# Kernel tuning notes

Hardware: AMD Instinct MI355X
Metric: run time of the kernel (lower is better)

The kernel has to match this reference:

```python
import jax, jax.numpy as jnp
import numpy as np

B, C, S, H, W = 2, 128, 64, 128, 512
MID = 32
EPS = 1e-5


def layer_norm(x, g, b):
    m = jnp.mean(x, axis=-1, keepdims=True)
    v = jnp.var(x, axis=-1, keepdims=True)
    return (x - m) / jnp.sqrt(v + EPS) * g + b


def generate_y_for_attn(s, y, u):
    # y: [B, Cy, H, W], u: [B, s, s] int indices into W (clamped)
    b, cy, h, w = y.shape
    u = jnp.clip(u, 0, w - 1)
    yr = y.reshape(b, cy * h, w)
    idx = u.reshape(b, s * s)
    g = jax.vmap(lambda m, i: m[:, i])(yr, idx)          # [B, Cy*H, s^2]
    return g.reshape(b, cy, h, s * s).transpose(0, 3, 2, 1)  # [B, s^2, H, Cy]


def setup_inputs():
    key = jax.random.key(0)
    ks = jax.random.split(key, 10)
    lim = 1.0 / np.sqrt(C)
    return {
        "sat_x": jax.random.normal(ks[0], (B, C, S, S), jnp.float32),
        "grd_x": jax.random.normal(ks[1], (B, C, H, W), jnp.float32),
        "grd_height": jax.random.normal(ks[2], (B, 1, H, W), jnp.float32),
        "u": jax.random.randint(ks[3], (B, S, S), 0, W, jnp.int32),
        "ln_q_g": jnp.ones((C,), jnp.float32),
        "ln_q_b": jnp.zeros((C,), jnp.float32),
        "wq": jax.random.uniform(ks[4], (C, MID), jnp.float32, -lim, lim),
        "bq": jax.random.uniform(ks[5], (MID,), jnp.float32, -lim, lim),
        "ln_k_g": jnp.ones((C,), jnp.float32),
        "ln_k_b": jnp.zeros((C,), jnp.float32),
        "wk": jax.random.uniform(ks[6], (C, MID), jnp.float32, -lim, lim),
        "bk": jax.random.uniform(ks[7], (MID,), jnp.float32, -lim, lim),
    }


def reference(sat_x, grd_x, grd_height, u, ln_q_g, ln_q_b, wq, bq, ln_k_g, ln_k_b, wk, bk):
    b, c, s, _ = sat_x.shape
    scale = MID ** (-0.5)
    y_attn = generate_y_for_attn(s, grd_x, u)        # [B, S^2, H, C]
    v_attn = generate_y_for_attn(s, grd_height, u)   # [B, S^2, H, 1]
    x = sat_x.reshape(b, c, s * s).transpose(0, 2, 1)  # [B, M, C]
    q = layer_norm(x, ln_q_g, ln_q_b) @ wq + bq        # [B, M, 32]
    k = layer_norm(y_attn, ln_k_g, ln_k_b) @ wk + bk   # [B, M, H, 32]
    dot = scale * jnp.einsum("bmd,bmnd->bmn", q, k)    # [B, M, H]
    att = jax.nn.softmax(dot, axis=-1)
    a = jnp.sum(att[..., None] * v_attn, axis=-2)      # [B, M, 1]
    return a.transpose(0, 2, 1).reshape(b, 1, s, s)
```

## Files before the change

kernel.cpp:

```cpp
#include <hip/hip_runtime.h>
#include <math.h>

#define B_   2
#define C_   128
#define S_   64
#define H_   128
#define W_   512
#define M_   (S_ * S_)
#define MID_ 32
#define EPS_ 1e-5f
#define CAP_ 192

#define KBLK (B_ * H_ * (W_ / 64))
#define QBLK (B_ * (M_ / 64))
#define NTILE (KBLK + QBLK)
#define PGRID 1024
#define OBLK 4

typedef __attribute__((ext_vector_type(8))) short short8;
typedef __attribute__((ext_vector_type(4))) float floatx4;

__device__ __forceinline__ unsigned bfpair(float a, float b) {
    unsigned ua = __float_as_uint(a); ua += 0x7FFFu + ((ua >> 16) & 1u);
    unsigned ub = __float_as_uint(b); ub += 0x7FFFu + ((ub >> 16) & 1u);
    return (ua >> 16) | (ub & 0xFFFF0000u);
}

__global__ __launch_bounds__(256) void prep_kernel(
    const float* __restrict__ ln_k_g, const float* __restrict__ ln_k_b,
    const float* __restrict__ wk, const float* __restrict__ bk,
    const float* __restrict__ ln_q_g, const float* __restrict__ ln_q_b,
    const float* __restrict__ wq, const float* __restrict__ bq,
    float* __restrict__ prepbuf,
    short* __restrict__ wfrag,
    int* __restrict__ counts,
    int* __restrict__ ocount)
{
    const int tid = threadIdx.x;
    const int blk = blockIdx.x;
    const float* g    = blk ? ln_q_g : ln_k_g;
    const float* bl   = blk ? ln_q_b : ln_k_b;
    const float* wt   = blk ? wq     : wk;
    const float* bias = blk ? bq     : bk;

    __shared__ float pa[256], pb[256];

    float a = 0.f, c2 = 0.f;
#pragma unroll
    for (int k = 0; k < 16; ++k) {
        const int idx = tid + 256 * k;
        const float wv = wt[idx];
        const int c = idx >> 5;
        a  = fmaf(g[c],  wv, a);
        c2 = fmaf(bl[c], wv, c2);
    }
    pa[tid] = a; pb[tid] = c2;

    if (blk == 0) {
        ((int4*)counts)[tid] = make_int4(0, 0, 0, 0);
        if (tid == 0) *ocount = 0;
    }
    __syncthreads();

    if (tid < 32) {
        float s = 0.f, t = 0.f;
#pragma unroll
        for (int r = 0; r < 8; ++r) { s += pa[tid + 32 * r]; t += pb[tid + 32 * r]; }
        prepbuf[blk * 64 + tid]      = s;
        prepbuf[blk * 64 + 32 + tid] = t + bias[tid];
    }

    short* whiT = wfrag + blk * 8192;
    short* wloT = whiT + 4096;
#pragma unroll
    for (int e = 0; e < 16; ++e) {
        const int idx = tid * 16 + e;
        const int i    = idx & 7;
        const int ln   = (idx >> 3) & 63;
        const int kk   = (idx >> 9) & 3;
        const int jt   = idx >> 11;
        const int c = kk * 32 + (ln >> 4) * 8 + i;
        const int j = jt * 16 + (ln & 15);
        const float wp = g[c] * wt[c * MID_ + j];
        const unsigned bbits = __float_as_uint(wp);
        const unsigned hb = bbits & 0xFFFF0000u;
        whiT[idx] = (short)(hb >> 16);
        const float r = wp - __uint_as_float(hb);
        wloT[idx] = (short)(__float_as_uint(r) >> 16);
    }
}

struct Geo {
    const float* xcol;
    size_t xstr;
    int b, h, pos0;
    bool is_k;
};

__device__ __forceinline__ Geo tile_geo(int t, const float* __restrict__ grd_x,
                                        const float* __restrict__ sat_x) {
    Geo ge;
    ge.is_k = (t < KBLK);
    if (ge.is_k) {
        const int wchunk = t & 7;
        ge.h    = (t >> 3) & (H_ - 1);
        ge.b    = t >> 10;
        ge.pos0 = wchunk * 64;
        ge.xcol = grd_x + ((size_t)ge.b * C_ * H_ + ge.h) * W_ + ge.pos0;
        ge.xstr = (size_t)H_ * W_;
    } else {
        const int qblk = t - KBLK;
        ge.b    = qblk >> 6;
        ge.h    = 0;
        ge.pos0 = (qblk & 63) * 64;
        ge.xcol = sat_x + (size_t)ge.b * C_ * M_ + ge.pos0;
        ge.xstr = (size_t)M_;
    }
    return ge;
}

__device__ __forceinline__ void issue_dma(const Geo& ge, float* xs, int lane, int wv) {
    const int swz  = (wv >> 1) << 4;
    const float* gsrc = ge.xcol + (size_t)(lane >> 4) * ge.xstr
                               + (((lane & 15) * 4) ^ swz);
#pragma unroll
    for (int r = 0; r < 8; ++r) {
        const float* src = gsrc + (size_t)(r * 16 + wv * 4) * ge.xstr;
        float* dst = xs + (r * 16 + wv * 4) * 64;
        __builtin_amdgcn_global_load_lds(
            (const __attribute__((address_space(1))) unsigned int*)src,
            (__attribute__((address_space(3))) unsigned int*)dst,
            16, 0, 0);
    }
}

__global__ __launch_bounds__(256) void proj_kernel(
    const float* __restrict__ grd_x,
    const float* __restrict__ sat_x,
    const float* __restrict__ prepbuf,
    const short* __restrict__ wfrag,
    const int*   __restrict__ u,
    unsigned short* __restrict__ kwb,
    float* __restrict__ qv,
    int* __restrict__ counts,
    int* __restrict__ bucket,
    int* __restrict__ ocount,
    int* __restrict__ olist)
{
    __shared__ float xs[C_ * 64];

    const int tid  = threadIdx.x;
    const int lane = tid & 63;
    const int wv   = __builtin_amdgcn_readfirstlane(tid >> 6);
    const int quad = lane >> 4;
    const int l16  = lane & 15;
    const int blk  = blockIdx.x;

    issue_dma(tile_geo(blk, grd_x, sat_x), xs, lane, wv);

    for (int t = blk; t < NTILE; t += PGRID) {
        const Geo ge = tile_geo(t, grd_x, sat_x);
        const bool is_k = ge.is_k;
        const int pos = ge.pos0 + wv * 16 + l16;

        const short* whiT = wfrag + (is_k ? 0 : 8192);
        const short* wloT = whiT + 4096;
        short8 ahi[2][4], alo[2][4];
#pragma unroll
        for (int jt = 0; jt < 2; ++jt)
#pragma unroll
            for (int kk = 0; kk < 4; ++kk) {
                const int off = ((jt * 4 + kk) * 64 + lane) * 8;
                ahi[jt][kk] = *(const short8*)(whiT + off);
                alo[jt][kk] = *(const short8*)(wloT + off);
            }

        const int setoff = is_k ? 0 : 64;
        const float4 gw0 = *(const float4*)(prepbuf + setoff + quad * 4);
        const float4 bw0 = *(const float4*)(prepbuf + setoff + 32 + quad * 4);
        const float4 gw1 = *(const float4*)(prepbuf + setoff + 16 + quad * 4);
        const float4 bw1 = *(const float4*)(prepbuf + setoff + 48 + quad * 4);

        __syncthreads();

        floatx4 acc0 = {0.f, 0.f, 0.f, 0.f};
        floatx4 acc1 = {0.f, 0.f, 0.f, 0.f};
        float p1 = 0.f, p2 = 0.f;

        const int rpos = (wv * 16 + l16) ^ ((quad & 1) << 4);
        const float* xsl = xs + quad * 8 * 64 + rpos;

#pragma unroll
        for (int kk = 0; kk < 4; ++kk) {
            const float* xk = xsl + kk * 32 * 64;
            union { short8 v; unsigned u[4]; } bhi, blo;
#pragma unroll
            for (int e = 0; e < 4; ++e) {
                const float x0 = xk[(2 * e)     * 64];
                const float x1 = xk[(2 * e + 1) * 64];
                p1 += x0 + x1;
                p2 = fmaf(x0, x0, p2);
                p2 = fmaf(x1, x1, p2);
                const unsigned b0 = __float_as_uint(x0);
                const unsigned b1 = __float_as_uint(x1);
                bhi.u[e] = (b1 & 0xFFFF0000u) | (b0 >> 16);
                const float r0 = x0 - __uint_as_float(b0 & 0xFFFF0000u);
                const float r1 = x1 - __uint_as_float(b1 & 0xFFFF0000u);
                blo.u[e] = (__float_as_uint(r1) & 0xFFFF0000u) |
                           (__float_as_uint(r0) >> 16);
            }
            acc0 = __builtin_amdgcn_mfma_f32_16x16x32_bf16(ahi[0][kk], bhi.v, acc0, 0, 0, 0);
            acc1 = __builtin_amdgcn_mfma_f32_16x16x32_bf16(ahi[1][kk], bhi.v, acc1, 0, 0, 0);
            acc0 = __builtin_amdgcn_mfma_f32_16x16x32_bf16(ahi[0][kk], blo.v, acc0, 0, 0, 0);
            acc1 = __builtin_amdgcn_mfma_f32_16x16x32_bf16(ahi[1][kk], blo.v, acc1, 0, 0, 0);
            acc0 = __builtin_amdgcn_mfma_f32_16x16x32_bf16(alo[0][kk], bhi.v, acc0, 0, 0, 0);
            acc1 = __builtin_amdgcn_mfma_f32_16x16x32_bf16(alo[1][kk], bhi.v, acc1, 0, 0, 0);
        }

        __syncthreads();
        if (t + PGRID < NTILE)
            issue_dma(tile_geo(t + PGRID, grd_x, sat_x), xs, lane, wv);

        p1 += __shfl_xor(p1, 16, 64);
        p1 += __shfl_xor(p1, 32, 64);
        p2 += __shfl_xor(p2, 16, 64);
        p2 += __shfl_xor(p2, 32, 64);
        const float mean = p1 * (1.f / C_);
        const float rstd = rsqrtf(fmaf(-mean, mean, p2 * (1.f / C_)) + EPS_);

        const float o0x = fmaf(rstd, fmaf(-mean, gw0.x, acc0[0]), bw0.x);
        const float o0y = fmaf(rstd, fmaf(-mean, gw0.y, acc0[1]), bw0.y);
        const float o0z = fmaf(rstd, fmaf(-mean, gw0.z, acc0[2]), bw0.z);
        const float o0w = fmaf(rstd, fmaf(-mean, gw0.w, acc0[3]), bw0.w);
        const float o1x = fmaf(rstd, fmaf(-mean, gw1.x, acc1[0]), bw1.x);
        const float o1y = fmaf(rstd, fmaf(-mean, gw1.y, acc1[1]), bw1.y);
        const float o1z = fmaf(rstd, fmaf(-mean, gw1.z, acc1[2]), bw1.z);
        const float o1w = fmaf(rstd, fmaf(-mean, gw1.w, acc1[3]), bw1.w);

        if (is_k) {
            unsigned short* orow = kwb + (((size_t)ge.b * W_ + pos) * H_ + ge.h) * MID_;
            uint2 u0, u1;
            u0.x = bfpair(o0x, o0y); u0.y = bfpair(o0z, o0w);
            u1.x = bfpair(o1x, o1y); u1.y = bfpair(o1z, o1w);
            *(uint2*)(orow + quad * 4)      = u0;
            *(uint2*)(orow + 16 + quad * 4) = u1;
        } else {
            float* orow = qv + ((size_t)ge.b * M_ + pos) * MID_;
            *(float4*)(orow + quad * 4)      = make_float4(o0x, o0y, o0z, o0w);
            *(float4*)(orow + 16 + quad * 4) = make_float4(o1x, o1y, o1z, o1w);
            if (quad == 0) {
                const int bm = ge.b * M_ + pos;
                int w = u[bm];
                w = min(max(w, 0), W_ - 1);
                const int bw = ge.b * W_ + w;
                const int p = atomicAdd(&counts[bw], 1);
                if (p < CAP_) bucket[bw * CAP_ + p] = bm;
                else          olist[atomicAdd(ocount, 1)] = bm;
            }
        }
    }
}

__global__ __launch_bounds__(256) void battn_kernel(
    const float* __restrict__ qv,
    const unsigned short* __restrict__ kwb,
    const float* __restrict__ gh,
    const int*   __restrict__ u,
    const int*   __restrict__ counts,
    const int*   __restrict__ bucket,
    const int*   __restrict__ ocount,
    const int*   __restrict__ olist,
    float* __restrict__ out)
{
    const int blk  = blockIdx.x;
    const int tid  = threadIdx.x;
    const int lane = tid & 63;
    const int wv   = __builtin_amdgcn_readfirstlane(tid >> 6);
    const float sc = 0.17677669529663687f;

    if (blk >= B_ * W_) {
        const int nof = min(*ocount, B_ * M_);
        const int gwv = (blk - B_ * W_) * 4 + wv;
        for (int i = gwv; i < nof; i += OBLK * 4) {
            const int bm = __builtin_amdgcn_readfirstlane(olist[i]);
            const int b  = bm >> 12;
            int w = u[bm];
            w = min(max(w, 0), W_ - 1);
            const unsigned short* kr = kwb + ((size_t)b * W_ + w) * H_ * MID_;
            const float* qr = qv + (size_t)bm * MID_;
            float sq[MID_];
#pragma unroll
            for (int j = 0; j < MID_; ++j) sq[j] = qr[j];
            float d0 = 0.f, d1 = 0.f;
#pragma unroll
            for (int j = 0; j < MID_; ++j) {
                d0 = fmaf(sq[j], __uint_as_float((unsigned)kr[lane * MID_ + j] << 16), d0);
                d1 = fmaf(sq[j], __uint_as_float((unsigned)kr[(lane + 64) * MID_ + j] << 16), d1);
            }
            d0 *= sc; d1 *= sc;
            float mx = fmaxf(d0, d1);
#pragma unroll
            for (int o = 32; o > 0; o >>= 1) mx = fmaxf(mx, __shfl_xor(mx, o, 64));
            const float v0 = gh[((size_t)b * H_ + lane) * W_ + w];
            const float v1 = gh[((size_t)b * H_ + lane + 64) * W_ + w];
            const float e0 = __expf(d0 - mx);
            const float e1 = __expf(d1 - mx);
            float s   = e0 + e1;
            float svv = fmaf(e0, v0, e1 * v1);
#pragma unroll
            for (int o = 32; o > 0; o >>= 1) {
                s   += __shfl_xor(s,   o, 64);
                svv += __shfl_xor(svv, o, 64);
            }
            if (lane == 0) out[bm] = svv / s;
        }
        return;
    }

    const int n = min(counts[blk], CAP_);
    if (wv >= n) return;

    const int b = blk >> 9;
    const int w = blk & (W_ - 1);

    const uint4* k4 = (const uint4*)(kwb + (size_t)blk * H_ * MID_);
    float ka[32], kb[32];
#pragma unroll
    for (int t = 0; t < 4; ++t) {
        const uint4 ua = k4[lane * 4 + t];
        const uint4 ub = k4[(lane + 64) * 4 + t];
        ka[t*8+0] = __uint_as_float(ua.x << 16); ka[t*8+1] = __uint_as_float(ua.x & 0xFFFF0000u);
        ka[t*8+2] = __uint_as_float(ua.y << 16); ka[t*8+3] = __uint_as_float(ua.y & 0xFFFF0000u);
        ka[t*8+4] = __uint_as_float(ua.z << 16); ka[t*8+5] = __uint_as_float(ua.z & 0xFFFF0000u);
        ka[t*8+6] = __uint_as_float(ua.w << 16); ka[t*8+7] = __uint_as_float(ua.w & 0xFFFF0000u);
        kb[t*8+0] = __uint_as_float(ub.x << 16); kb[t*8+1] = __uint_as_float(ub.x & 0xFFFF0000u);
        kb[t*8+2] = __uint_as_float(ub.y << 16); kb[t*8+3] = __uint_as_float(ub.y & 0xFFFF0000u);
        kb[t*8+4] = __uint_as_float(ub.z << 16); kb[t*8+5] = __uint_as_float(ub.z & 0xFFFF0000u);
        kb[t*8+6] = __uint_as_float(ub.w << 16); kb[t*8+7] = __uint_as_float(ub.w & 0xFFFF0000u);
    }

    const float v0 = gh[((size_t)b * H_ + lane) * W_ + w];
    const float v1 = gh[((size_t)b * H_ + lane + 64) * W_ + w];

    const int* bkt = bucket + (size_t)blk * CAP_;

    for (int i = wv; i < n; i += 4) {
        const int bm = __builtin_amdgcn_readfirstlane(bkt[i]);
        const float* qr = qv + (size_t)bm * MID_;
        float sq[MID_];
#pragma unroll
        for (int j = 0; j < MID_; ++j) sq[j] = qr[j];

        float d0 = 0.f, d1 = 0.f;
#pragma unroll
        for (int j = 0; j < MID_; ++j) {
            d0 = fmaf(sq[j], ka[j], d0);
            d1 = fmaf(sq[j], kb[j], d1);
        }
        d0 *= sc; d1 *= sc;

        float mx = fmaxf(d0, d1);
#pragma unroll
        for (int o = 32; o > 0; o >>= 1) mx = fmaxf(mx, __shfl_xor(mx, o, 64));

        const float e0 = __expf(d0 - mx);
        const float e1 = __expf(d1 - mx);
        float s   = e0 + e1;
        float svv = fmaf(e0, v0, e1 * v1);
#pragma unroll
        for (int o = 32; o > 0; o >>= 1) {
            s   += __shfl_xor(s,   o, 64);
            svv += __shfl_xor(svv, o, 64);
        }

        if (lane == 0) out[bm] = svv / s;
    }
}

extern "C" void kernel_launch(void* const* d_in, const int* in_sizes, int n_in,
                              void* d_out, int out_size, void* d_ws, size_t ws_size,
                              hipStream_t stream) {
    const float* sat_x      = (const float*)d_in[0];
    const float* grd_x      = (const float*)d_in[1];
    const float* grd_height = (const float*)d_in[2];
    const int*   u          = (const int*)d_in[3];
    const float* ln_q_g     = (const float*)d_in[4];
    const float* ln_q_b     = (const float*)d_in[5];
    const float* wq         = (const float*)d_in[6];
    const float* bq         = (const float*)d_in[7];
    const float* ln_k_g     = (const float*)d_in[8];
    const float* ln_k_b     = (const float*)d_in[9];
    const float* wk         = (const float*)d_in[10];
    const float* bk         = (const float*)d_in[11];

    float* out = (float*)d_out;

    char* ws = (char*)d_ws;
    unsigned short* kwb = (unsigned short*)ws;
    float* q       = (float*)(ws + (size_t)8  * 1024 * 1024);
    int*   counts  = (int*)  (ws + (size_t)9  * 1024 * 1024);
    int*   ocount  = (int*)  (ws + (size_t)9  * 1024 * 1024 + 4096);
    int*   bucket  = (int*)  (ws + (size_t)9  * 1024 * 1024 + 8192);
    int*   olist   = bucket + B_ * W_ * CAP_;
    float* prepbuf = (float*)(ws + (size_t)10 * 1024 * 1024);
    short* wfrag   = (short*)(ws + (size_t)10 * 1024 * 1024 + 4096);

    prep_kernel<<<2, 256, 0, stream>>>(
        ln_k_g, ln_k_b, wk, bk, ln_q_g, ln_q_b, wq, bq,
        prepbuf, wfrag, counts, ocount);
    proj_kernel<<<PGRID, 256, 0, stream>>>(
        grd_x, sat_x, prepbuf, wfrag, u, kwb, q, counts, bucket, ocount, olist);
    battn_kernel<<<B_ * W_ + OBLK, 256, 0, stream>>>(
        q, kwb, grd_height, u, counts, bucket, ocount, olist, out);
}
```

Before: 135.5 us.

## Fold weight prep into projection kernel and launch one block per tile

```diff
diff --git a/kernel.cpp b/kernel.cpp
--- a/kernel.cpp
+++ b/kernel.cpp
@@ -14,7 +14,6 @@
 #define KBLK (B_ * H_ * (W_ / 64))
 #define QBLK (B_ * (M_ / 64))
 #define NTILE (KBLK + QBLK)
-#define PGRID 1024
 #define OBLK 4
 
 typedef __attribute__((ext_vector_type(8))) short short8;
@@ -24,70 +23,6 @@
     unsigned ua = __float_as_uint(a); ua += 0x7FFFu + ((ua >> 16) & 1u);
     unsigned ub = __float_as_uint(b); ub += 0x7FFFu + ((ub >> 16) & 1u);
     return (ua >> 16) | (ub & 0xFFFF0000u);
-}
-
-__global__ __launch_bounds__(256) void prep_kernel(
-    const float* __restrict__ ln_k_g, const float* __restrict__ ln_k_b,
-    const float* __restrict__ wk, const float* __restrict__ bk,
-    const float* __restrict__ ln_q_g, const float* __restrict__ ln_q_b,
-    const float* __restrict__ wq, const float* __restrict__ bq,
-    float* __restrict__ prepbuf,
-    short* __restrict__ wfrag,
-    int* __restrict__ counts,
-    int* __restrict__ ocount)
-{
-    const int tid = threadIdx.x;
-    const int blk = blockIdx.x;
-    const float* g    = blk ? ln_q_g : ln_k_g;
-    const float* bl   = blk ? ln_q_b : ln_k_b;
-    const float* wt   = blk ? wq     : wk;
-    const float* bias = blk ? bq     : bk;
-
-    __shared__ float pa[256], pb[256];
-
-    float a = 0.f, c2 = 0.f;
-#pragma unroll
-    for (int k = 0; k < 16; ++k) {
-        const int idx = tid + 256 * k;
-        const float wv = wt[idx];
-        const int c = idx >> 5;
-        a  = fmaf(g[c],  wv, a);
-        c2 = fmaf(bl[c], wv, c2);
-    }
-    pa[tid] = a; pb[tid] = c2;
-
-    if (blk == 0) {
-        ((int4*)counts)[tid] = make_int4(0, 0, 0, 0);
-        if (tid == 0) *ocount = 0;
-    }
-    __syncthreads();
-
-    if (tid < 32) {
-        float s = 0.f, t = 0.f;
-#pragma unroll
-        for (int r = 0; r < 8; ++r) { s += pa[tid + 32 * r]; t += pb[tid + 32 * r]; }
-        prepbuf[blk * 64 + tid]      = s;
-        prepbuf[blk * 64 + 32 + tid] = t + bias[tid];
-    }
-
-    short* whiT = wfrag + blk * 8192;
-    short* wloT = whiT + 4096;
-#pragma unroll
-    for (int e = 0; e < 16; ++e) {
-        const int idx = tid * 16 + e;
-        const int i    = idx & 7;
-        const int ln   = (idx >> 3) & 63;
-        const int kk   = (idx >> 9) & 3;
-        const int jt   = idx >> 11;
-        const int c = kk * 32 + (ln >> 4) * 8 + i;
-        const int j = jt * 16 + (ln & 15);
-        const float wp = g[c] * wt[c * MID_ + j];
-        const unsigned bbits = __float_as_uint(wp);
-        const unsigned hb = bbits & 0xFFFF0000u;
-        whiT[idx] = (short)(hb >> 16);
-        const float r = wp - __uint_as_float(hb);
-        wloT[idx] = (short)(__float_as_uint(r) >> 16);
-    }
 }
 
 struct Geo {
@@ -137,8 +72,10 @@
 __global__ __launch_bounds__(256) void proj_kernel(
     const float* __restrict__ grd_x,
     const float* __restrict__ sat_x,
-    const float* __restrict__ prepbuf,
-    const short* __restrict__ wfrag,
+    const float* __restrict__ ln_k_g, const float* __restrict__ ln_k_b,
+    const float* __restrict__ wk, const float* __restrict__ bk,
+    const float* __restrict__ ln_q_g, const float* __restrict__ ln_q_b,
+    const float* __restrict__ wq, const float* __restrict__ bq,
     const int*   __restrict__ u,
     unsigned short* __restrict__ kwb,
     float* __restrict__ qv,
@@ -155,108 +92,136 @@
     const int quad = lane >> 4;
     const int l16  = lane & 15;
     const int blk  = blockIdx.x;
-
-    issue_dma(tile_geo(blk, grd_x, sat_x), xs, lane, wv);
-
-    for (int t = blk; t < NTILE; t += PGRID) {
-        const Geo ge = tile_geo(t, grd_x, sat_x);
-        const bool is_k = ge.is_k;
-        const int pos = ge.pos0 + wv * 16 + l16;
-
-        const short* whiT = wfrag + (is_k ? 0 : 8192);
-        const short* wloT = whiT + 4096;
-        short8 ahi[2][4], alo[2][4];
-#pragma unroll
-        for (int jt = 0; jt < 2; ++jt)
-#pragma unroll
-            for (int kk = 0; kk < 4; ++kk) {
-                const int off = ((jt * 4 + kk) * 64 + lane) * 8;
-                ahi[jt][kk] = *(const short8*)(whiT + off);
-                alo[jt][kk] = *(const short8*)(wloT + off);
+    const bool is_k = (blk < KBLK);
+
+    const Geo ge = tile_geo(blk, grd_x, sat_x);
+    const int pos = ge.pos0 + wv * 16 + l16;
+
+    issue_dma(ge, xs, lane, wv);
+
+    const float* g    = is_k ? ln_k_g : ln_q_g;
+    const float* beta = is_k ? ln_k_b : ln_q_b;
+    const float* wt   = is_k ? wk     : wq;
+    const float* bias = is_k ? bk     : bq;
+
+    short8 ahi[2][4], alo[2][4];
+    float gwp0 = 0.f, gwp1 = 0.f, bwp0 = 0.f, bwp1 = 0.f;
+#pragma unroll
+    for (int kk = 0; kk < 4; ++kk) {
+#pragma unroll
+        for (int i = 0; i < 8; ++i) {
+            const int c   = kk * 32 + quad * 8 + i;
+            const float gc = g[c];
+            const float bc = beta[c];
+            {
+                const float w0 = wt[c * MID_ + l16];
+                const float wp = gc * w0;
+                const unsigned hb = __float_as_uint(wp) & 0xFFFF0000u;
+                ahi[0][kk][i] = (short)(hb >> 16);
+                const float r = wp - __uint_as_float(hb);
+                alo[0][kk][i] = (short)(__float_as_uint(r) >> 16);
+                gwp0 += wp;
+                bwp0 = fmaf(bc, w0, bwp0);
             }
-
-        const int setoff = is_k ? 0 : 64;
-        const float4 gw0 = *(const float4*)(prepbuf + setoff + quad * 4);
-        const float4 bw0 = *(const float4*)(prepbuf + setoff + 32 + quad * 4);
-        const float4 gw1 = *(const float4*)(prepbuf + setoff + 16 + quad * 4);
-        const float4 bw1 = *(const float4*)(prepbuf + setoff + 48 + quad * 4);
-
-        __syncthreads();
-
-        floatx4 acc0 = {0.f, 0.f, 0.f, 0.f};
-        floatx4 acc1 = {0.f, 0.f, 0.f, 0.f};
-        float p1 = 0.f, p2 = 0.f;
-
-        const int rpos = (wv * 16 + l16) ^ ((quad & 1) << 4);
-        const float* xsl = xs + quad * 8 * 64 + rpos;
-
-#pragma unroll
-        for (int kk = 0; kk < 4; ++kk) {
-            const float* xk = xsl + kk * 32 * 64;
-            union { short8 v; unsigned u[4]; } bhi, blo;
-#pragma unroll
-            for (int e = 0; e < 4; ++e) {
-                const float x0 = xk[(2 * e)     * 64];
-                const float x1 = xk[(2 * e + 1) * 64];
-                p1 += x0 + x1;
-                p2 = fmaf(x0, x0, p2);
-                p2 = fmaf(x1, x1, p2);
-                const unsigned b0 = __float_as_uint(x0);
-                const unsigned b1 = __float_as_uint(x1);
-                bhi.u[e] = (b1 & 0xFFFF0000u) | (b0 >> 16);
-                const float r0 = x0 - __uint_as_float(b0 & 0xFFFF0000u);
-                const float r1 = x1 - __uint_as_float(b1 & 0xFFFF0000u);
-                blo.u[e] = (__float_as_uint(r1) & 0xFFFF0000u) |
-                           (__float_as_uint(r0) >> 16);
+            {
+                const float w1 = wt[c * MID_ + 16 + l16];
+                const float wp = gc * w1;
+                const unsigned hb = __float_as_uint(wp) & 0xFFFF0000u;
+                ahi[1][kk][i] = (short)(hb >> 16);
+                const float r = wp - __uint_as_float(hb);
+                alo[1][kk][i] = (short)(__float_as_uint(r) >> 16);
+                gwp1 += wp;
+                bwp1 = fmaf(bc, w1, bwp1);
             }
-            acc0 = __builtin_amdgcn_mfma_f32_16x16x32_bf16(ahi[0][kk], bhi.v, acc0, 0, 0, 0);
-            acc1 = __builtin_amdgcn_mfma_f32_16x16x32_bf16(ahi[1][kk], bhi.v, acc1, 0, 0, 0);
-            acc0 = __builtin_amdgcn_mfma_f32_16x16x32_bf16(ahi[0][kk], blo.v, acc0, 0, 0, 0);
-            acc1 = __builtin_amdgcn_mfma_f32_16x16x32_bf16(ahi[1][kk], blo.v, acc1, 0, 0, 0);
-            acc0 = __builtin_amdgcn_mfma_f32_16x16x32_bf16(alo[0][kk], bhi.v, acc0, 0, 0, 0);
-            acc1 = __builtin_amdgcn_mfma_f32_16x16x32_bf16(alo[1][kk], bhi.v, acc1, 0, 0, 0);
-        }
-
-        __syncthreads();
-        if (t + PGRID < NTILE)
-            issue_dma(tile_geo(t + PGRID, grd_x, sat_x), xs, lane, wv);
-
-        p1 += __shfl_xor(p1, 16, 64);
-        p1 += __shfl_xor(p1, 32, 64);
-        p2 += __shfl_xor(p2, 16, 64);
-        p2 += __shfl_xor(p2, 32, 64);
-        const float mean = p1 * (1.f / C_);
-        const float rstd = rsqrtf(fmaf(-mean, mean, p2 * (1.f / C_)) + EPS_);
-
-        const float o0x = fmaf(rstd, fmaf(-mean, gw0.x, acc0[0]), bw0.x);
-        const float o0y = fmaf(rstd, fmaf(-mean, gw0.y, acc0[1]), bw0.y);
-        const float o0z = fmaf(rstd, fmaf(-mean, gw0.z, acc0[2]), bw0.z);
-        const float o0w = fmaf(rstd, fmaf(-mean, gw0.w, acc0[3]), bw0.w);
-        const float o1x = fmaf(rstd, fmaf(-mean, gw1.x, acc1[0]), bw1.x);
-        const float o1y = fmaf(rstd, fmaf(-mean, gw1.y, acc1[1]), bw1.y);
-        const float o1z = fmaf(rstd, fmaf(-mean, gw1.z, acc1[2]), bw1.z);
-        const float o1w = fmaf(rstd, fmaf(-mean, gw1.w, acc1[3]), bw1.w);
-
-        if (is_k) {
-            unsigned short* orow = kwb + (((size_t)ge.b * W_ + pos) * H_ + ge.h) * MID_;
-            uint2 u0, u1;
-            u0.x = bfpair(o0x, o0y); u0.y = bfpair(o0z, o0w);
-            u1.x = bfpair(o1x, o1y); u1.y = bfpair(o1z, o1w);
-            *(uint2*)(orow + quad * 4)      = u0;
-            *(uint2*)(orow + 16 + quad * 4) = u1;
-        } else {
-            float* orow = qv + ((size_t)ge.b * M_ + pos) * MID_;
-            *(float4*)(orow + quad * 4)      = make_float4(o0x, o0y, o0z, o0w);
-            *(float4*)(orow + 16 + quad * 4) = make_float4(o1x, o1y, o1z, o1w);
-            if (quad == 0) {
-                const int bm = ge.b * M_ + pos;
-                int w = u[bm];
-                w = min(max(w, 0), W_ - 1);
-                const int bw = ge.b * W_ + w;
-                const int p = atomicAdd(&counts[bw], 1);
-                if (p < CAP_) bucket[bw * CAP_ + p] = bm;
-                else          olist[atomicAdd(ocount, 1)] = bm;
-            }
+        }
+    }
+    gwp0 += __shfl_xor(gwp0, 16, 64); gwp0 += __shfl_xor(gwp0, 32, 64);
+    gwp1 += __shfl_xor(gwp1, 16, 64); gwp1 += __shfl_xor(gwp1, 32, 64);
+    bwp0 += __shfl_xor(bwp0, 16, 64); bwp0 += __shfl_xor(bwp0, 32, 64);
+    bwp1 += __shfl_xor(bwp1, 16, 64); bwp1 += __shfl_xor(bwp1, 32, 64);
+    bwp0 += bias[l16];
+    bwp1 += bias[16 + l16];
+    float4 gw0, gw1, bw0, bw1;
+    gw0.x = __shfl(gwp0, quad * 4 + 0, 64); gw0.y = __shfl(gwp0, quad * 4 + 1, 64);
+    gw0.z = __shfl(gwp0, quad * 4 + 2, 64); gw0.w = __shfl(gwp0, quad * 4 + 3, 64);
+    gw1.x = __shfl(gwp1, quad * 4 + 0, 64); gw1.y = __shfl(gwp1, quad * 4 + 1, 64);
+    gw1.z = __shfl(gwp1, quad * 4 + 2, 64); gw1.w = __shfl(gwp1, quad * 4 + 3, 64);
+    bw0.x = __shfl(bwp0, quad * 4 + 0, 64); bw0.y = __shfl(bwp0, quad * 4 + 1, 64);
+    bw0.z = __shfl(bwp0, quad * 4 + 2, 64); bw0.w = __shfl(bwp0, quad * 4 + 3, 64);
+    bw1.x = __shfl(bwp1, quad * 4 + 0, 64); bw1.y = __shfl(bwp1, quad * 4 + 1, 64);
+    bw1.z = __shfl(bwp1, quad * 4 + 2, 64); bw1.w = __shfl(bwp1, quad * 4 + 3, 64);
+
+    __syncthreads();
+
+    floatx4 acc0 = {0.f, 0.f, 0.f, 0.f};
+    floatx4 acc1 = {0.f, 0.f, 0.f, 0.f};
+    float p1 = 0.f, p2 = 0.f;
+
+    const int rpos = (wv * 16 + l16) ^ ((quad & 1) << 4);
+    const float* xsl = xs + quad * 8 * 64 + rpos;
+
+#pragma unroll
+    for (int kk = 0; kk < 4; ++kk) {
+        const float* xk = xsl + kk * 32 * 64;
+        union { short8 v; unsigned u[4]; } bhi, blo;
+#pragma unroll
+        for (int e = 0; e < 4; ++e) {
+            const float x0 = xk[(2 * e)     * 64];
+            const float x1 = xk[(2 * e + 1) * 64];
+            p1 += x0 + x1;
+            p2 = fmaf(x0, x0, p2);
+            p2 = fmaf(x1, x1, p2);
+            const unsigned b0 = __float_as_uint(x0);
+            const unsigned b1 = __float_as_uint(x1);
+            bhi.u[e] = (b1 & 0xFFFF0000u) | (b0 >> 16);
+            const float r0 = x0 - __uint_as_float(b0 & 0xFFFF0000u);
+            const float r1 = x1 - __uint_as_float(b1 & 0xFFFF0000u);
+            blo.u[e] = (__float_as_uint(r1) & 0xFFFF0000u) |
+                       (__float_as_uint(r0) >> 16);
+        }
+        acc0 = __builtin_amdgcn_mfma_f32_16x16x32_bf16(ahi[0][kk], bhi.v, acc0, 0, 0, 0);
+        acc1 = __builtin_amdgcn_mfma_f32_16x16x32_bf16(ahi[1][kk], bhi.v, acc1, 0, 0, 0);
+        acc0 = __builtin_amdgcn_mfma_f32_16x16x32_bf16(ahi[0][kk], blo.v, acc0, 0, 0, 0);
+        acc1 = __builtin_amdgcn_mfma_f32_16x16x32_bf16(ahi[1][kk], blo.v, acc1, 0, 0, 0);
+        acc0 = __builtin_amdgcn_mfma_f32_16x16x32_bf16(alo[0][kk], bhi.v, acc0, 0, 0, 0);
+        acc1 = __builtin_amdgcn_mfma_f32_16x16x32_bf16(alo[1][kk], bhi.v, acc1, 0, 0, 0);
+    }
+
+    p1 += __shfl_xor(p1, 16, 64);
+    p1 += __shfl_xor(p1, 32, 64);
+    p2 += __shfl_xor(p2, 16, 64);
+    p2 += __shfl_xor(p2, 32, 64);
+    const float mean = p1 * (1.f / C_);
+    const float rstd = rsqrtf(fmaf(-mean, mean, p2 * (1.f / C_)) + EPS_);
+
+    const float o0x = fmaf(rstd, fmaf(-mean, gw0.x, acc0[0]), bw0.x);
+    const float o0y = fmaf(rstd, fmaf(-mean, gw0.y, acc0[1]), bw0.y);
+    const float o0z = fmaf(rstd, fmaf(-mean, gw0.z, acc0[2]), bw0.z);
+    const float o0w = fmaf(rstd, fmaf(-mean, gw0.w, acc0[3]), bw0.w);
+    const float o1x = fmaf(rstd, fmaf(-mean, gw1.x, acc1[0]), bw1.x);
+    const float o1y = fmaf(rstd, fmaf(-mean, gw1.y, acc1[1]), bw1.y);
+    const float o1z = fmaf(rstd, fmaf(-mean, gw1.z, acc1[2]), bw1.z);
+    const float o1w = fmaf(rstd, fmaf(-mean, gw1.w, acc1[3]), bw1.w);
+
+    if (is_k) {
+        unsigned short* orow = kwb + (((size_t)ge.b * W_ + pos) * H_ + ge.h) * MID_;
+        uint2 u0, u1;
+        u0.x = bfpair(o0x, o0y); u0.y = bfpair(o0z, o0w);
+        u1.x = bfpair(o1x, o1y); u1.y = bfpair(o1z, o1w);
+        *(uint2*)(orow + quad * 4)      = u0;
+        *(uint2*)(orow + 16 + quad * 4) = u1;
+    } else {
+        float* orow = qv + ((size_t)ge.b * M_ + pos) * MID_;
+        *(float4*)(orow + quad * 4)      = make_float4(o0x, o0y, o0z, o0w);
+        *(float4*)(orow + 16 + quad * 4) = make_float4(o1x, o1y, o1z, o1w);
+        if (quad == 0) {
+            const int bm = ge.b * M_ + pos;
+            int w = u[bm];
+            w = min(max(w, 0), W_ - 1);
+            const int bw = ge.b * W_ + w;
+            const int p = atomicAdd(&counts[bw], 1);
+            if (p < CAP_) bucket[bw * CAP_ + p] = bm;
+            else          olist[atomicAdd(ocount, 1)] = bm;
         }
     }
 }
@@ -282,7 +247,7 @@
         const int nof = min(*ocount, B_ * M_);
         const int gwv = (blk - B_ * W_) * 4 + wv;
         for (int i = gwv; i < nof; i += OBLK * 4) {
-            const int bm = __builtin_amdgcn_readfirstlane(olist[i]);
+            const int bm = olist[i];
             const int b  = bm >> 12;
             int w = u[bm];
             w = min(max(w, 0), W_ - 1);
@@ -345,7 +310,7 @@
     const int* bkt = bucket + (size_t)blk * CAP_;
 
     for (int i = wv; i < n; i += 4) {
-        const int bm = __builtin_amdgcn_readfirstlane(bkt[i]);
+        const int bm = bkt[i];
         const float* qr = qv + (size_t)bm * MID_;
         float sq[MID_];
 #pragma unroll
@@ -402,14 +367,14 @@
     int*   ocount  = (int*)  (ws + (size_t)9  * 1024 * 1024 + 4096);
     int*   bucket  = (int*)  (ws + (size_t)9  * 1024 * 1024 + 8192);
     int*   olist   = bucket + B_ * W_ * CAP_;
-    float* prepbuf = (float*)(ws + (size_t)10 * 1024 * 1024);
-    short* wfrag   = (short*)(ws + (size_t)10 * 1024 * 1024 + 4096);
-
-    prep_kernel<<<2, 256, 0, stream>>>(
-        ln_k_g, ln_k_b, wk, bk, ln_q_g, ln_q_b, wq, bq,
-        prepbuf, wfrag, counts, ocount);
-    proj_kernel<<<PGRID, 256, 0, stream>>>(
-        grd_x, sat_x, prepbuf, wfrag, u, kwb, q, counts, bucket, ocount, olist);
+
+    hipMemsetAsync(counts, 0, 8192, stream);
+
+    proj_kernel<<<NTILE, 256, 0, stream>>>(
+        grd_x, sat_x,
+        ln_k_g, ln_k_b, wk, bk,
+        ln_q_g, ln_q_b, wq, bq,
+        u, kwb, q, counts, bucket, ocount, olist);
     battn_kernel<<<B_ * W_ + OBLK, 256, 0, stream>>>(
         q, kwb, grd_height, u, counts, bucket, ocount, olist, out);
 }
```

Measured after the change: 137.5 us. About the same (+1.5%).
